# Performance work log

Hardware: AMD Instinct MI355X
Metric: run time of the kernel (lower is better)

Reference implementation:

```python
import jax, jax.numpy as jnp
import numpy as np

FP8_MAX = 448.0  # max normal of float8_e4m3fn
NUM_HEADS = 16


def act_quant(x):
    # per-tensor fp8 quantization: scale so max|x| maps to FP8_MAX
    scale = jnp.max(jnp.abs(x)) / FP8_MAX
    q = (x / scale).astype(jnp.float8_e4m3fn)
    return q, scale


def setup_inputs() -> dict:
    key = jax.random.key(0)
    k1, k2, k3, k4 = jax.random.split(key, 4)
    B, S, H = 2, 2048, 2048
    x = jax.random.normal(k1, (B, S, H), dtype=jnp.float32)
    W_qkv = jax.random.normal(k2, (H, 3 * H), dtype=jnp.float32) * (1.0 / np.sqrt(H))
    W_out = jax.random.normal(k3, (H, H), dtype=jnp.float32) * (1.0 / np.sqrt(H))
    b_out = jnp.zeros((H,), dtype=jnp.float32)
    return {"x": x, "W_qkv": W_qkv, "W_out": W_out, "b_out": b_out}


def reference(x, W_qkv, W_out, b_out):
    B, S, H = x.shape
    nH = NUM_HEADS
    hd = H // nH  # 128, matches head_dim default used for scaling

    qkv = jnp.einsum('bsh,hf->bsf', x, W_qkv)          # [B,S,3H]
    qkv = qkv.reshape(B, S, 3, nH, hd)
    q = qkv[:, :, 0].transpose(0, 2, 1, 3)             # [B,nH,S,hd]
    k = qkv[:, :, 1].transpose(0, 2, 1, 3)
    v = qkv[:, :, 2].transpose(0, 2, 1, 3)

    q8, q_scale = act_quant(q)
    k8, k_scale = act_quant(k)
    # fp8_gemm_optimized: dequantized GEMM = (a @ b) * a_scale * b_scale
    scores = jnp.einsum('bhqd,bhkd->bhqk',
                        q8.astype(jnp.float32), k8.astype(jnp.float32))
    scores = scores * (q_scale * k_scale) / jnp.sqrt(jnp.float32(hd))

    attn = jax.nn.softmax(scores, axis=-1)             # [B,nH,S,S]
    # (dropout omitted: deterministic / eval mode)

    v8, v_scale = act_quant(v)
    out = jnp.einsum('bhqk,bhkd->bhqd', attn, v8.astype(jnp.float32))
    out = out * v_scale                                # a_scale = 1 for attn weights

    out = out.transpose(0, 2, 1, 3).reshape(B, S, H)
    return jnp.einsum('bsh,ho->bso', out, W_out) + b_out
```

## Files before the change

### kernel.cpp

```cpp
#include <hip/hip_runtime.h>
#include <hip/hip_bf16.h>
#include <math.h>

#define B_   2
#define S_   2048
#define H_   2048
#define NH   16
#define HD   128
#define ROWS (B_ * S_)
#define F3   (3 * H_)
#define KS   2048

typedef _Float16 f16x8 __attribute__((ext_vector_type(8)));
typedef float    f32x4  __attribute__((ext_vector_type(4)));
typedef float    f32x16 __attribute__((ext_vector_type(16)));

union H2 { unsigned u; _Float16 h[2]; };
union H4 { ushort4 s4; _Float16 h[4]; };
union H4b { uint2 u2; _Float16 h[4]; };
union PU { unsigned u[4]; f16x8 v8; };

__device__ __forceinline__ void gl_lds16(const void* g, void* l) {
  __builtin_amdgcn_global_load_lds(
      (const __attribute__((address_space(1))) void*)g,
      (__attribute__((address_space(3))) void*)l, 16, 0, 0);
}

__device__ __forceinline__ float quant_e4m3(float x) {
  float ax = fabsf(x);
  float q;
  if (ax < 0.015625f) {
    q = rintf(ax * 512.0f) * (1.0f / 512.0f);
  } else {
    unsigned eb = __float_as_uint(ax) & 0x7f800000u;
    float quantum = __uint_as_float(eb - (3u << 23));
    q = rintf(ax / quantum) * quantum;
    if (q > 448.0f) q = 448.0f;
  }
  return copysignf(q, x);
}

__global__ __launch_bounds__(256) void split_ab(
    const float* __restrict__ in, _Float16* __restrict__ hi,
    _Float16* __restrict__ lo) {
  const size_t i = (size_t)blockIdx.x * 256 + threadIdx.x;
  float4 v = ((const float4*)in)[i];
  H4 h, l;
  h.h[0] = (_Float16)v.x; l.h[0] = (_Float16)(v.x - (float)h.h[0]);
  h.h[1] = (_Float16)v.y; l.h[1] = (_Float16)(v.y - (float)h.h[1]);
  h.h[2] = (_Float16)v.z; l.h[2] = (_Float16)(v.z - (float)h.h[2]);
  h.h[3] = (_Float16)v.w; l.h[3] = (_Float16)(v.w - (float)h.h[3]);
  ((ushort4*)hi)[i] = h.s4;
  ((ushort4*)lo)[i] = l.s4;
}

__global__ __launch_bounds__(256) void split_tr(
    const float* __restrict__ in, _Float16* __restrict__ hi,
    _Float16* __restrict__ lo, int K, int N) {
  __shared__ _Float16 ht[64][72];
  __shared__ _Float16 lt[64][72];
  const int t = threadIdx.x;
  const int n0 = blockIdx.x * 64, k0 = blockIdx.y * 64;
#pragma unroll
  for (int p = 0; p < 4; p++) {
    const int k = p * 16 + (t >> 4);
    const int n = (t & 15) * 4;
    float4 v = *(const float4*)(in + (size_t)(k0 + k) * N + n0 + n);
    _Float16 h0 = (_Float16)v.x, h1 = (_Float16)v.y,
             h2 = (_Float16)v.z, h3 = (_Float16)v.w;
    ht[n + 0][k] = h0; lt[n + 0][k] = (_Float16)(v.x - (float)h0);
    ht[n + 1][k] = h1; lt[n + 1][k] = (_Float16)(v.y - (float)h1);
    ht[n + 2][k] = h2; lt[n + 2][k] = (_Float16)(v.z - (float)h2);
    ht[n + 3][k] = h3; lt[n + 3][k] = (_Float16)(v.w - (float)h3);
  }
  __syncthreads();
#pragma unroll
  for (int it = 0; it < 2; it++) {
    const int idx = it * 256 + t;
    const int r = idx >> 3, c = (idx & 7) * 8;
    *(uint4*)(hi + (size_t)(n0 + r) * K + k0 + c) = *(const uint4*)&ht[r][c];
    *(uint4*)(lo + (size_t)(n0 + r) * K + k0 + c) = *(const uint4*)&lt[r][c];
  }
}

#define STAGE_A(tt, dst) do {                                                  \
    const _Float16* As_ = ((tt) < 64) ? Ahi : Alo;                             \
    const size_t so_ = (size_t)(row0 + wave * 8 + srow) * KS +                 \
                       (((tt) & 31) << 6) + schunk;                            \
    _Float16* db_ = (dst) + wave * 512;                                        \
    gl_lds16(As_ + so_,                    db_);                               \
    gl_lds16(As_ + so_ + (size_t)64 * KS,  db_ + 4096);                        \
    gl_lds16(As_ + so_ + (size_t)128 * KS, db_ + 8192);                       \
    gl_lds16(As_ + so_ + (size_t)192 * KS, db_ + 12288);                       \
  } while (0)

#define STAGE_B(tt, dst) do {                                                  \
    const _Float16* Bs_ = ((((tt) >> 5)) == 1) ? Btlo : Bthi;                  \
    const size_t so_ = (size_t)(col0 + wave * 8 + srow) * KS +                 \
                       (((tt) & 31) << 6) + schunk;                            \
    _Float16* db_ = (dst) + 16384 + wave * 512;                                \
    gl_lds16(Bs_ + so_,                    db_);                               \
    gl_lds16(Bs_ + so_ + (size_t)64 * KS,  db_ + 4096);                        \
  } while (0)

__global__ __launch_bounds__(512, 2) void gemm_split256(
    const _Float16* __restrict__ Ahi, const _Float16* __restrict__ Alo,
    const _Float16* __restrict__ Bthi, const _Float16* __restrict__ Btlo,
    float* __restrict__ C, const float* __restrict__ bias,
    unsigned* mx, int N, int has_bias) {
  __shared__ __align__(16) _Float16 lds[73728];
  const int t = threadIdx.x;
  const int wave = t >> 6, lane = t & 63;
  const int l15 = lane & 15, g = lane >> 4;
  const int wm = wave >> 1, wn = wave & 1;

  const int gx = gridDim.x;
  const int nwg = gx * gridDim.y;
  const int bid = blockIdx.y * gx + blockIdx.x;
  const int tile = (bid & 7) * (nwg >> 3) + (bid >> 3);
  const int row0 = (tile / gx) * 256, col0 = (tile % gx) * 128;

  const int srow = lane >> 3;
  const int schunk = ((lane & 7) ^ srow) << 3;

  f32x4 acc[4][4] = {};

  _Float16* bufA = lds;
  _Float16* bufB = lds + 24576;
  _Float16* bufC = lds + 49152;

  STAGE_A(0, bufA);
  STAGE_B(0, bufA);
  STAGE_A(1, bufB);
  STAGE_B(1, bufB);
  asm volatile("s_waitcnt vmcnt(6)" ::: "memory");
  __builtin_amdgcn_s_barrier();

  for (int kc = 0; kc < 96; kc++) {
    const _Float16* Ab = bufA;
    const _Float16* Bb = bufA + 16384;
    f16x8 af0[4], bf0[4], af1[4], bf1[4];
#pragma unroll
    for (int i = 0; i < 4; i++) {
      const int r_ = wm * 64 + i * 16 + l15;
      af0[i] = *(const f16x8*)(Ab + r_ * 64 + ((g ^ (r_ & 7)) << 3));
      af1[i] = *(const f16x8*)(Ab + r_ * 64 + (((4 ^ g) ^ (r_ & 7)) << 3));
    }
#pragma unroll
    for (int j = 0; j < 4; j++) {
      const int r_ = wn * 64 + j * 16 + l15;
      bf0[j] = *(const f16x8*)(Bb + r_ * 64 + ((g ^ (r_ & 7)) << 3));
      bf1[j] = *(const f16x8*)(Bb + r_ * 64 + (((4 ^ g) ^ (r_ & 7)) << 3));
    }
    if (kc + 2 < 96) {
      STAGE_A(kc + 2, bufC);
      STAGE_B(kc + 2, bufC);
    }
#pragma unroll
    for (int i = 0; i < 4; i++)
#pragma unroll
      for (int j = 0; j < 4; j++)
        acc[i][j] = __builtin_amdgcn_mfma_f32_16x16x32_f16(af0[i], bf0[j], acc[i][j], 0, 0, 0);
#pragma unroll
    for (int i = 0; i < 4; i++)
#pragma unroll
      for (int j = 0; j < 4; j++)
        acc[i][j] = __builtin_amdgcn_mfma_f32_16x16x32_f16(af1[i], bf1[j], acc[i][j], 0, 0, 0);
    if (kc < 94) { asm volatile("s_waitcnt vmcnt(6)" ::: "memory"); }
    else         { asm volatile("s_waitcnt vmcnt(0)" ::: "memory"); }
    __builtin_amdgcn_s_barrier();
    _Float16* tmp = bufA; bufA = bufB; bufB = bufC; bufC = tmp;
  }

  float bmax = 0.0f;
#pragma unroll
  for (int j = 0; j < 4; j++) {
    const int col = col0 + wn * 64 + j * 16 + l15;
    const float bv = has_bias ? bias[col] : 0.0f;
#pragma unroll
    for (int i = 0; i < 4; i++) {
      const int rbase = row0 + wm * 64 + i * 16 + g * 4;
#pragma unroll
      for (int r = 0; r < 4; r++) {
        const float v = acc[i][j][r] + bv;
        C[(size_t)(rbase + r) * N + col] = v;
        bmax = fmaxf(bmax, fabsf(v));
      }
    }
  }

  if (mx) {
    __syncthreads();
    float* red = (float*)lds;
    red[t] = bmax;
    __syncthreads();
    for (int s2 = 256; s2 > 0; s2 >>= 1) {
      if (t < s2) red[t] = fmaxf(red[t], red[t + s2]);
      __syncthreads();
    }
    if (t == 0) atomicMax(mx + (col0 >> 11), __float_as_uint(red[0]));
  }
}

__global__ __launch_bounds__(256) void quant_qkv(
    const float* __restrict__ qkv, const unsigned* __restrict__ mx,
    _Float16* __restrict__ q8, _Float16* __restrict__ k8,
    _Float16* __restrict__ v8t) {
  __shared__ _Float16 tile[64 * 72];
  const int t = threadIdx.x;
  const int bid = blockIdx.x;

  if (bid < 16384) {
    const size_t base = ((size_t)bid * 256 + t) * 4;
    const int row = (int)(base >> 12);
    const int col = (int)(base & 4095);
    const int seg = col >> 11;
    const int c2 = col & 2047;
    const int h = c2 >> 7, d = c2 & 127;
    const int b = row >> 11, s = row & 2047;
    const float scale = __uint_as_float(mx[seg]) / 448.0f;
    float4 v = *(const float4*)(qkv + (size_t)row * F3 + col);
    H4 r;
    r.h[0] = (_Float16)quant_e4m3(v.x / scale);
    r.h[1] = (_Float16)quant_e4m3(v.y / scale);
    r.h[2] = (_Float16)quant_e4m3(v.z / scale);
    r.h[3] = (_Float16)quant_e4m3(v.w / scale);
    _Float16* dst = seg ? k8 : q8;
    const size_t di = ((size_t)((b * NH + h) * S_) + s) * HD + d;
    *(ushort4*)(dst + di) = r.s4;
  } else {
    const int bt = bid - 16384;
    const int dtile = bt & 1;
    const int stile = (bt >> 1) & 31;
    const int bh = bt >> 6;
    const int b = bh >> 4, h = bh & 15;
    const int s0 = stile * 64, d0 = dtile * 64;
    const float scale = __uint_as_float(mx[2]) / 448.0f;

#pragma unroll
    for (int r = 0; r < 4; r++) {
      const int s = s0 + r * 16 + (t >> 4);
      const int dl = (t & 15) * 4;
      float4 v = *(const float4*)(qkv + (size_t)(b * S_ + s) * F3 + 4096 + h * HD + d0 + dl);
      tile[(dl + 0) * 72 + r * 16 + (t >> 4)] = (_Float16)quant_e4m3(v.x / scale);
      tile[(dl + 1) * 72 + r * 16 + (t >> 4)] = (_Float16)quant_e4m3(v.y / scale);
      tile[(dl + 2) * 72 + r * 16 + (t >> 4)] = (_Float16)quant_e4m3(v.z / scale);
      tile[(dl + 3) * 72 + r * 16 + (t >> 4)] = (_Float16)quant_e4m3(v.w / scale);
    }
    __syncthreads();
#pragma unroll
    for (int j = 0; j < 2; j++) {
      const int wi = j * 256 + t;
      const int dl = wi >> 3;
      const int sch = (wi & 7) * 8;
      uint4 val = *(const uint4*)(tile + dl * 72 + sch);
      *(uint4*)(v8t + (size_t)bh * (HD * S_) + (size_t)(d0 + dl) * S_ + s0 + sch) = val;
    }
  }
}

__global__ __launch_bounds__(256, 2) void attn_kernel(
    const _Float16* __restrict__ q8, const _Float16* __restrict__ k8,
    const _Float16* __restrict__ v8t, const unsigned* __restrict__ mx,
    _Float16* __restrict__ oHi, _Float16* __restrict__ oLo) {
  __shared__ __align__(16) char ldsb[65536];

  const int t = threadIdx.x;
  const int wave = t >> 6;
  const int lane = t & 63;
  const int l31 = lane & 31;
  const int hf = lane >> 5;

  const int qt = blockIdx.x & 15;
  const int bh = blockIdx.x >> 4;
  const int b = bh >> 4, h = bh & 15;
  const int q0 = qt * 128 + wave * 32;

  const float qs = __uint_as_float(mx[0]) * (1.0f / 448.0f);
  const float ks = __uint_as_float(mx[1]) * (1.0f / 448.0f);
  const float vs = __uint_as_float(mx[2]) * (1.0f / 448.0f);
  const float sfac = qs * ks * 0.08838834764831843f;

  f16x8 qf[8];
  {
    const _Float16* qp = q8 + ((size_t)(bh * S_) + q0 + l31) * HD + hf * 8;
#pragma unroll
    for (int st = 0; st < 8; st++)
      qf[st] = *(const f16x8*)(qp + st * 16);
  }

  f32x16 acc[4] = {};
  float m_base = 0.0f;
  float l_run = 0.0f;

  const size_t kB_ = (size_t)(bh * S_) * HD;
  const size_t vB_ = (size_t)bh * (HD * S_);
  const int k_key = t >> 4;
  const int k_dch = (t & 15) * 8;
  const int k_wch = (((t & 15) ^ (k_key & 7)) << 3);
  const int v_d   = t >> 3;
  const int v_sch = (t & 7) * 8;
  const int v_wch = (((t & 7) ^ (v_d & 7)) << 3);

  const int NT = S_ / 64;
  uint4 kp[4], vp[4];

#pragma unroll
  for (int r = 0; r < 4; r++)
    kp[r] = *(const uint4*)(k8 + kB_ + (size_t)(r * 16 + k_key) * HD + k_dch);
#pragma unroll
  for (int r = 0; r < 4; r++)
    vp[r] = *(const uint4*)(v8t + vB_ + (size_t)(r * 32 + v_d) * S_ + v_sch);
  {
    _Float16* K0 = (_Float16*)ldsb;
    _Float16* V0 = (_Float16*)(ldsb + 32768);
#pragma unroll
    for (int r = 0; r < 4; r++)
      *(uint4*)(K0 + (r * 16 + k_key) * 128 + k_wch) = kp[r];
#pragma unroll
    for (int r = 0; r < 4; r++)
      *(uint4*)(V0 + (r * 32 + v_d) * 64 + v_wch) = vp[r];
  }
#pragma unroll
  for (int r = 0; r < 4; r++)
    kp[r] = *(const uint4*)(k8 + kB_ + (size_t)(64 + r * 16 + k_key) * HD + k_dch);
#pragma unroll
  for (int r = 0; r < 4; r++)
    vp[r] = *(const uint4*)(v8t + vB_ + (size_t)(r * 32 + v_d) * S_ + 64 + v_sch);
  __syncthreads();

  for (int kt = 0; kt < NT; kt++) {
    const _Float16* Klds  = (const _Float16*)(ldsb + (kt & 1) * 16384);
    const _Float16* VTlds = (const _Float16*)(ldsb + 32768 + (kt & 1) * 16384);
    if (kt + 1 < NT) {
      _Float16* Kn = (_Float16*)(ldsb + ((kt + 1) & 1) * 16384);
      _Float16* Vn = (_Float16*)(ldsb + 32768 + ((kt + 1) & 1) * 16384);
#pragma unroll
      for (int r = 0; r < 4; r++)
        *(uint4*)(Kn + (r * 16 + k_key) * 128 + k_wch) = kp[r];
#pragma unroll
      for (int r = 0; r < 4; r++)
        *(uint4*)(Vn + (r * 32 + v_d) * 64 + v_wch) = vp[r];
    }
    if (kt + 2 < NT) {
      const int nk = (kt + 2) * 64;
#pragma unroll
      for (int r = 0; r < 4; r++)
        kp[r] = *(const uint4*)(k8 + kB_ + (size_t)(nk + r * 16 + k_key) * HD + k_dch);
#pragma unroll
      for (int r = 0; r < 4; r++)
        vp[r] = *(const uint4*)(v8t + vB_ + (size_t)(r * 32 + v_d) * S_ + nk + v_sch);
    }

#pragma unroll
    for (int sub = 0; sub < 2; sub++) {
      const int ksub = sub * 32;
      f32x16 s = {};
      __builtin_amdgcn_s_setprio(1);
#pragma unroll
      for (int st = 0; st < 8; st++) {
        const int krow = ksub + l31;
        f16x8 af = *(const f16x8*)(Klds + krow * 128 +
                                   (((st * 2 + hf) ^ (krow & 7)) << 3));
        s = __builtin_amdgcn_mfma_f32_32x32x16_f16(af, qf[st], s, 0, 0, 0);
      }
      __builtin_amdgcn_s_setprio(0);
      f16x8 vf0 = *(const f16x8*)(VTlds + l31 * 64 +
                                  (((sub * 4 + 0 * 2 + hf) ^ (l31 & 7)) << 3));
      f16x8 vf1 = *(const f16x8*)(VTlds + l31 * 64 +
                                  (((sub * 4 + 1 * 2 + hf) ^ (l31 & 7)) << 3));
      float p[16];
      if (kt == 0 && sub == 0) {
        float tmax = -3.0e38f;
#pragma unroll
        for (int i = 0; i < 16; i++) {
          p[i] = s[i] * sfac;
          tmax = fmaxf(tmax, p[i]);
        }
        tmax = fmaxf(tmax, __shfl_xor(tmax, 32));
        m_base = tmax;
        float rs = 0.0f;
#pragma unroll
        for (int i = 0; i < 16; i++) {
          p[i] = __expf(p[i] - tmax);
          rs += p[i];
        }
        l_run += rs;
      } else {
        const float mb = m_base;
        float rs = 0.0f;
#pragma unroll
        for (int i = 0; i < 16; i++) {
          p[i] = fminf(__expf(fmaf(s[i], sfac, -mb)), 60000.0f);
          rs += p[i];
        }
        l_run += rs;
      }
      f16x8 pf[2];
#pragma unroll
      for (int c = 0; c < 2; c++) {
        const int c8 = c * 8;
        const int sidx = hf ? 0 : 4;
        const int oidx = hf ? 4 : 0;
        H2 s0h, s1h, o0h, o1h;
        s0h.h[0] = (_Float16)p[c8 + sidx];     s0h.h[1] = (_Float16)p[c8 + sidx + 1];
        s1h.h[0] = (_Float16)p[c8 + sidx + 2]; s1h.h[1] = (_Float16)p[c8 + sidx + 3];
        o0h.h[0] = (_Float16)p[c8 + oidx];     o0h.h[1] = (_Float16)p[c8 + oidx + 1];
        o1h.h[0] = (_Float16)p[c8 + oidx + 2]; o1h.h[1] = (_Float16)p[c8 + oidx + 3];
        unsigned r0 = (unsigned)__shfl_xor((int)s0h.u, 32);
        unsigned r1 = (unsigned)__shfl_xor((int)s1h.u, 32);
        PU pu;
        if (hf == 0) { pu.u[0] = o0h.u; pu.u[1] = o1h.u; pu.u[2] = r0; pu.u[3] = r1; }
        else         { pu.u[0] = r0;    pu.u[1] = r1;    pu.u[2] = o0h.u; pu.u[3] = o1h.u; }
        pf[c] = pu.v8;
      }
#pragma unroll
      for (int dt = 0; dt < 4; dt++) {
        f16x8 nf0, nf1;
        if (dt < 3) {
          const int vrow = (dt + 1) * 32 + l31;
          nf0 = *(const f16x8*)(VTlds + vrow * 64 +
                                (((sub * 4 + 0 * 2 + hf) ^ (vrow & 7)) << 3));
          nf1 = *(const f16x8*)(VTlds + vrow * 64 +
                                (((sub * 4 + 1 * 2 + hf) ^ (vrow & 7)) << 3));
        }
        __builtin_amdgcn_s_setprio(1);
        acc[dt] = __builtin_amdgcn_mfma_f32_32x32x16_f16(vf0, pf[0], acc[dt], 0, 0, 0);
        acc[dt] = __builtin_amdgcn_mfma_f32_32x32x16_f16(vf1, pf[1], acc[dt], 0, 0, 0);
        __builtin_amdgcn_s_setprio(0);
        vf0 = nf0; vf1 = nf1;
      }
    }
    __syncthreads();
  }

  l_run += __shfl_xor(l_run, 32);
  const float f = vs / l_run;

  _Float16* obuf = (_Float16*)ldsb;
  const int obase = wave * 4352;
#pragma unroll
  for (int pass = 0; pass < 2; pass++) {
    __syncthreads();
#pragma unroll
    for (int dt = 0; dt < 4; dt++) {
#pragma unroll
      for (int iq = 0; iq < 4; iq++) {
        const int dl0 = 8 * iq + 4 * hf;
        H4b w;
#pragma unroll
        for (int e = 0; e < 4; e++) {
          const float o = acc[dt][iq * 4 + e] * f;
          const _Float16 hh = (_Float16)o;
          w.h[e] = pass ? (_Float16)(o - (float)hh) : hh;
        }
        *(uint2*)&obuf[obase + l31 * 136 + dt * 32 + dl0] = w.u2;
      }
    }
    __syncthreads();
    _Float16* dst = pass ? oLo : oHi;
#pragma unroll
    for (int ii = 0; ii < 8; ii++) {
      const int qrow = ii * 4 + (lane >> 4);
      const int ch = (lane & 15) * 8;
      uint4 val = *(const uint4*)&obuf[obase + qrow * 136 + ch];
      const size_t ofs = (size_t)(b * S_ + q0 + qrow) * H_ + h * HD + ch;
      *(uint4*)(dst + ofs) = val;
    }
  }
}

extern "C" void kernel_launch(void* const* d_in, const int* in_sizes, int n_in,
                              void* d_out, int out_size, void* d_ws, size_t ws_size,
                              hipStream_t stream) {
  const float* x     = (const float*)d_in[0];
  const float* W_qkv = (const float*)d_in[1];
  const float* W_out = (const float*)d_in[2];
  const float* b_out = (const float*)d_in[3];
  float* out = (float*)d_out;

  char* ws = (char*)d_ws;
  float*    qkv    = (float*)ws;
  _Float16* A2hi   = (_Float16*)(ws + 33554432);
  _Float16* A2lo   = (_Float16*)(ws + 50331648);
  _Float16* B2thi  = (_Float16*)(ws + 67108864);
  _Float16* B2tlo  = (_Float16*)(ws + 75497472);
  _Float16* B1thi  = (_Float16*)(ws + 100663296);
  _Float16* B1tlo  = (_Float16*)(ws + 125829120);
  _Float16* q8     = (_Float16*)(ws + 100663296);
  _Float16* k8     = (_Float16*)(ws + 117440512);
  _Float16* v8t    = (_Float16*)(ws + 134217728);
  _Float16* A1hi   = (_Float16*)(ws + 150994944);
  _Float16* A1lo   = (_Float16*)(ws + 167772160);
  unsigned* mx     = (unsigned*)(ws + 184549376);

  hipMemsetAsync(mx, 0, 3 * sizeof(unsigned), stream);

  split_ab<<<(ROWS * H_) / 1024, 256, 0, stream>>>(x, A1hi, A1lo);
  split_tr<<<dim3(F3 / 64, H_ / 64), 256, 0, stream>>>(W_qkv, B1thi, B1tlo, H_, F3);

  gemm_split256<<<dim3(F3 / 128, ROWS / 256), 512, 0, stream>>>(
      A1hi, A1lo, B1thi, B1tlo, qkv, nullptr, mx, F3, 0);

  quant_qkv<<<16384 + B_ * NH * 32 * 2, 256, 0, stream>>>(qkv, mx, q8, k8, v8t);

  attn_kernel<<<B_ * NH * 16, 256, 0, stream>>>(q8, k8, v8t, mx, A2hi, A2lo);

  split_tr<<<dim3(H_ / 64, H_ / 64), 256, 0, stream>>>(W_out, B2thi, B2tlo, H_, H_);

  gemm_split256<<<dim3(H_ / 128, ROWS / 256), 512, 0, stream>>>(
      A2hi, A2lo, B2thi, B2tlo, out, b_out, nullptr, H_, 1);
}
```

Baseline: 777.2 us.

## Merge input split kernels and interleave GEMM LDS loads with MFMA phases

Merges the x hi/lo split and the W_qkv transposed split into one launch, with block-index branching, to remove one kernel launch. The GEMM main loop is also reworked into two half-phases. Each phase reads one k-half of fragments from LDS and issues one operand's global-to-LDS stage. Barriers, sched_barrier and s_setprio then lift MFMA priority so waves alternate between memory and matrix work. This adds more barriers per iteration and may raise synchronization overhead.

```diff
diff --git a/kernel.cpp b/kernel.cpp
--- a/kernel.cpp
+++ b/kernel.cpp
@@ -40,18 +40,49 @@
   return copysignf(q, x);
 }
 
-__global__ __launch_bounds__(256) void split_ab(
-    const float* __restrict__ in, _Float16* __restrict__ hi,
-    _Float16* __restrict__ lo) {
-  const size_t i = (size_t)blockIdx.x * 256 + threadIdx.x;
-  float4 v = ((const float4*)in)[i];
-  H4 h, l;
-  h.h[0] = (_Float16)v.x; l.h[0] = (_Float16)(v.x - (float)h.h[0]);
-  h.h[1] = (_Float16)v.y; l.h[1] = (_Float16)(v.y - (float)h.h[1]);
-  h.h[2] = (_Float16)v.z; l.h[2] = (_Float16)(v.z - (float)h.h[2]);
-  h.h[3] = (_Float16)v.w; l.h[3] = (_Float16)(v.w - (float)h.h[3]);
-  ((ushort4*)hi)[i] = h.s4;
-  ((ushort4*)lo)[i] = l.s4;
+__global__ __launch_bounds__(256) void prep_split(
+    const float* __restrict__ x, const float* __restrict__ Wqkv,
+    _Float16* __restrict__ A1hi, _Float16* __restrict__ A1lo,
+    _Float16* __restrict__ B1thi, _Float16* __restrict__ B1tlo) {
+  __shared__ _Float16 ht[64][72];
+  __shared__ _Float16 lt[64][72];
+  const int t = threadIdx.x;
+  const int bid = blockIdx.x;
+  if (bid < 8192) {
+    const size_t i = (size_t)bid * 256 + t;
+    float4 v = ((const float4*)x)[i];
+    H4 h, l;
+    h.h[0] = (_Float16)v.x; l.h[0] = (_Float16)(v.x - (float)h.h[0]);
+    h.h[1] = (_Float16)v.y; l.h[1] = (_Float16)(v.y - (float)h.h[1]);
+    h.h[2] = (_Float16)v.z; l.h[2] = (_Float16)(v.z - (float)h.h[2]);
+    h.h[3] = (_Float16)v.w; l.h[3] = (_Float16)(v.w - (float)h.h[3]);
+    ((ushort4*)A1hi)[i] = h.s4;
+    ((ushort4*)A1lo)[i] = l.s4;
+  } else {
+    const int idx = bid - 8192;
+    const int n0 = (idx % 96) * 64, k0 = (idx / 96) * 64;
+    const int K = H_, N = F3;
+#pragma unroll
+    for (int p = 0; p < 4; p++) {
+      const int k = p * 16 + (t >> 4);
+      const int n = (t & 15) * 4;
+      float4 v = *(const float4*)(Wqkv + (size_t)(k0 + k) * N + n0 + n);
+      _Float16 h0 = (_Float16)v.x, h1 = (_Float16)v.y,
+               h2 = (_Float16)v.z, h3 = (_Float16)v.w;
+      ht[n + 0][k] = h0; lt[n + 0][k] = (_Float16)(v.x - (float)h0);
+      ht[n + 1][k] = h1; lt[n + 1][k] = (_Float16)(v.y - (float)h1);
+      ht[n + 2][k] = h2; lt[n + 2][k] = (_Float16)(v.z - (float)h2);
+      ht[n + 3][k] = h3; lt[n + 3][k] = (_Float16)(v.w - (float)h3);
+    }
+    __syncthreads();
+#pragma unroll
+    for (int it = 0; it < 2; it++) {
+      const int idx2 = it * 256 + t;
+      const int r = idx2 >> 3, c = (idx2 & 7) * 8;
+      *(uint4*)(B1thi + (size_t)(n0 + r) * K + k0 + c) = *(const uint4*)&ht[r][c];
+      *(uint4*)(B1tlo + (size_t)(n0 + r) * K + k0 + c) = *(const uint4*)&lt[r][c];
+    }
+  }
 }
 
 __global__ __launch_bounds__(256) void split_tr(
@@ -139,33 +170,51 @@
   for (int kc = 0; kc < 96; kc++) {
     const _Float16* Ab = bufA;
     const _Float16* Bb = bufA + 16384;
-    f16x8 af0[4], bf0[4], af1[4], bf1[4];
+    f16x8 af0[4], bf0[4];
 #pragma unroll
     for (int i = 0; i < 4; i++) {
       const int r_ = wm * 64 + i * 16 + l15;
       af0[i] = *(const f16x8*)(Ab + r_ * 64 + ((g ^ (r_ & 7)) << 3));
-      af1[i] = *(const f16x8*)(Ab + r_ * 64 + (((4 ^ g) ^ (r_ & 7)) << 3));
     }
 #pragma unroll
     for (int j = 0; j < 4; j++) {
       const int r_ = wn * 64 + j * 16 + l15;
       bf0[j] = *(const f16x8*)(Bb + r_ * 64 + ((g ^ (r_ & 7)) << 3));
-      bf1[j] = *(const f16x8*)(Bb + r_ * 64 + (((4 ^ g) ^ (r_ & 7)) << 3));
-    }
-    if (kc + 2 < 96) {
-      STAGE_A(kc + 2, bufC);
-      STAGE_B(kc + 2, bufC);
-    }
+    }
+    if (kc + 2 < 96) STAGE_A(kc + 2, bufC);
+    __builtin_amdgcn_s_barrier();
+    asm volatile("s_waitcnt lgkmcnt(0)" ::: "memory");
+    __builtin_amdgcn_sched_barrier(0);
+    __builtin_amdgcn_s_setprio(1);
 #pragma unroll
     for (int i = 0; i < 4; i++)
 #pragma unroll
       for (int j = 0; j < 4; j++)
         acc[i][j] = __builtin_amdgcn_mfma_f32_16x16x32_f16(af0[i], bf0[j], acc[i][j], 0, 0, 0);
+    __builtin_amdgcn_s_setprio(0);
+    __builtin_amdgcn_s_barrier();
+    f16x8 af1[4], bf1[4];
+#pragma unroll
+    for (int i = 0; i < 4; i++) {
+      const int r_ = wm * 64 + i * 16 + l15;
+      af1[i] = *(const f16x8*)(Ab + r_ * 64 + (((4 ^ g) ^ (r_ & 7)) << 3));
+    }
+#pragma unroll
+    for (int j = 0; j < 4; j++) {
+      const int r_ = wn * 64 + j * 16 + l15;
+      bf1[j] = *(const f16x8*)(Bb + r_ * 64 + (((4 ^ g) ^ (r_ & 7)) << 3));
+    }
+    if (kc + 2 < 96) STAGE_B(kc + 2, bufC);
+    __builtin_amdgcn_s_barrier();
+    asm volatile("s_waitcnt lgkmcnt(0)" ::: "memory");
+    __builtin_amdgcn_sched_barrier(0);
+    __builtin_amdgcn_s_setprio(1);
 #pragma unroll
     for (int i = 0; i < 4; i++)
 #pragma unroll
       for (int j = 0; j < 4; j++)
         acc[i][j] = __builtin_amdgcn_mfma_f32_16x16x32_f16(af1[i], bf1[j], acc[i][j], 0, 0, 0);
+    __builtin_amdgcn_s_setprio(0);
     if (kc < 94) { asm volatile("s_waitcnt vmcnt(6)" ::: "memory"); }
     else         { asm volatile("s_waitcnt vmcnt(0)" ::: "memory"); }
     __builtin_amdgcn_s_barrier();
@@ -496,8 +545,7 @@
 
   hipMemsetAsync(mx, 0, 3 * sizeof(unsigned), stream);
 
-  split_ab<<<(ROWS * H_) / 1024, 256, 0, stream>>>(x, A1hi, A1lo);
-  split_tr<<<dim3(F3 / 64, H_ / 64), 256, 0, stream>>>(W_qkv, B1thi, B1tlo, H_, F3);
+  prep_split<<<11264, 256, 0, stream>>>(x, W_qkv, A1hi, A1lo, B1thi, B1tlo);
 
   gemm_split256<<<dim3(F3 / 128, ROWS / 256), 512, 0, stream>>>(
       A1hi, A1lo, B1thi, B1tlo, qkv, nullptr, mx, F3, 0);
```

Result: no change. 784.4 us (+0.9%).
